# Kernel optimization log

Measured on AMD Instinct MI355X. Metric: run time of the kernel, lower is better.

## Reference

```python
import jax, jax.numpy as jnp
import numpy as np

K_BASE = 8
K_MAX = 20
NUM_GROUPS = 16  # min(32, 64 // 4)
EPS = 1e-5


def _knn_idx_adaptive(x, mask, k_base=K_BASE, k_max=K_MAX):
    # x: [B, N, D] float, mask: [B, N] bool. Returns idx: [B, N, k_max] int32.
    B, N, D = x.shape
    x2 = jnp.sum(x * x, axis=-1, keepdims=True)              # [B, N, 1]
    dist2 = x2 + x2.transpose(0, 2, 1) - 2.0 * jnp.einsum('bnd,bmd->bnm', x, x)
    dist2 = jnp.clip(dist2, 0.0)
    valid = mask[:, :, None] & mask[:, None, :]
    eye = jnp.eye(N, dtype=bool)[None]
    dist2 = jnp.where(valid & ~eye, dist2, jnp.inf)
    counts = mask.sum(axis=1)                                 # [B]
    k_per = jnp.clip(jnp.sqrt(counts.astype(jnp.float32) / 50.0) * k_base,
                     k_base, k_max).astype(jnp.int32)         # truncation == torch .long()
    k_global = jnp.minimum(k_max, jnp.maximum(1, counts.min() - 1))
    _, idx = jax.lax.top_k(-dist2, k_max)                     # [B, N, k_max]
    first_valid = jnp.argmax(mask, axis=1)                    # [B]
    cols = jnp.arange(k_max)[None, None, :]
    k_eff = jnp.minimum(k_per, k_global)[:, None, None]
    # cols < k_eff: true top-k neighbors; [k_eff, k_global): repeat first valid; >= k_global: pad 0
    idx = jnp.where(cols < k_eff, idx,
                    jnp.where(cols < k_global, first_valid[:, None, None], 0))
    return idx


def _group_norm(h, gamma, beta, num_groups=NUM_GROUPS, eps=EPS):
    # h: [..., C]
    shp = h.shape
    C = shp[-1]
    hg = h.reshape(shp[:-1] + (num_groups, C // num_groups))
    mu = hg.mean(axis=-1, keepdims=True)
    var = hg.var(axis=-1, keepdims=True)
    hg = (hg - mu) * jax.lax.rsqrt(var + eps)
    return hg.reshape(shp) * gamma + beta


def setup_inputs() -> dict:
    key = jax.random.key(0)
    kx, kl, k1, k2 = jax.random.split(key, 4)
    B, N, D, C = 16, 1024, 64, 64
    x = jax.random.normal(kx, (B, N, D), dtype=jnp.float32)
    lengths = jax.random.randint(kl, (B,), 256, N + 1)
    mask = jnp.arange(N)[None, :] < lengths[:, None]          # [B, N] bool
    W1 = jax.random.normal(k1, (2 * D, C), dtype=jnp.float32) / np.sqrt(2 * D)
    b1 = jnp.zeros((C,), dtype=jnp.float32)
    gamma = jnp.ones((C,), dtype=jnp.float32)
    beta = jnp.zeros((C,), dtype=jnp.float32)
    W2 = jax.random.normal(k2, (C, C), dtype=jnp.float32) / np.sqrt(C)
    b2 = jnp.zeros((C,), dtype=jnp.float32)
    return {"x": x, "mask": mask, "W1": W1, "b1": b1,
            "gamma": gamma, "beta": beta, "W2": W2, "b2": b2}


def reference(x, mask, W1, b1, gamma, beta, W2, b2):
    B, N, D = x.shape
    idx = _knn_idx_adaptive(x, mask)                          # [B, N, k]
    k = idx.shape[-1]
    x_nb = jnp.take_along_axis(x[:, :, None, :].repeat(1, axis=2),
                               idx[..., None], axis=1) if False else \
        x[jnp.arange(B)[:, None, None], idx]                  # [B, N, k, D]
    x_i = jnp.broadcast_to(x[:, :, None, :], (B, N, k, D))
    edge = jnp.concatenate([x_i, x_nb - x_i], axis=-1)        # [B, N, k, 2D]
    h = jax.nn.relu(_group_norm(edge @ W1 + b1, gamma, beta)) # [B, N, k, C]
    h = h @ W2 + b2
    out = h.max(axis=2)                                       # [B, N, C]
    return out * mask[..., None].astype(out.dtype)
```

## Files before the change

### kernel.cpp

```cpp
#include <hip/hip_runtime.h>
#include <stdint.h>

#define BB 16
#define NN 1024
#define DD 64
#define CC 64
#define KMAX 20
#define ROWS 8

typedef unsigned long long u64;
typedef float f32x2 __attribute__((ext_vector_type(2)));
typedef float f32x4v __attribute__((ext_vector_type(4)));
typedef short bf16x8 __attribute__((ext_vector_type(8)));

__device__ inline u64 umin64(u64 a, u64 b) { return a < b ? a : b; }

__device__ inline unsigned f2bf(float f) {
    unsigned u = __float_as_uint(f);
    return (u + 0x7FFFu + ((u >> 16) & 1u)) >> 16;
}

__device__ inline bf16x8 pack8(const float4 a, const float4 b) {
    union { unsigned u[4]; bf16x8 v; } r;
    r.u[0] = f2bf(a.x) | (f2bf(a.y) << 16);
    r.u[1] = f2bf(a.z) | (f2bf(a.w) << 16);
    r.u[2] = f2bf(b.x) | (f2bf(b.y) << 16);
    r.u[3] = f2bf(b.z) | (f2bf(b.w) << 16);
    return r.v;
}

struct bfpair { bf16x8 hi, lo; };
__device__ __forceinline__ bfpair split8(const float v[8]) {
    union { unsigned u[4]; bf16x8 x; } H, L;
#pragma unroll
    for (int i = 0; i < 4; ++i) {
        unsigned h0 = f2bf(v[2 * i]), h1 = f2bf(v[2 * i + 1]);
        float r0 = v[2 * i] - __uint_as_float(h0 << 16);
        float r1 = v[2 * i + 1] - __uint_as_float(h1 << 16);
        H.u[i] = h0 | (h1 << 16);
        L.u[i] = f2bf(r0) | (f2bf(r1) << 16);
    }
    bfpair r; r.hi = H.x; r.lo = L.x; return r;
}

__device__ inline void gn4(float4& h, const float4 g, const float4 be) {
    float mu = (h.x + h.y + h.z + h.w) * 0.25f;
    float dx = h.x - mu, dy = h.y - mu, dz = h.z - mu, dw = h.w - mu;
    float var = (dx * dx + dy * dy + dz * dz + dw * dw) * 0.25f;
    float rs = __builtin_amdgcn_rsqf(var + 1e-5f);
    h.x = fmaxf(fmaf(dx * rs, g.x, be.x), 0.f);
    h.y = fmaxf(fmaf(dy * rs, g.y, be.y), 0.f);
    h.z = fmaxf(fmaf(dz * rs, g.z, be.z), 0.f);
    h.w = fmaxf(fmaf(dw * rs, g.w, be.w), 0.f);
}

__global__ __launch_bounds__(256) void k1_feats(const float* __restrict__ x,
                                                const float* __restrict__ W1,
                                                const float* __restrict__ b1,
                                                float* __restrict__ base,
                                                float* __restrict__ fb,
                                                float* __restrict__ x2,
                                                float* __restrict__ xT,
                                                const void* __restrict__ maskp,
                                                int* __restrict__ counts,
                                                int* __restrict__ keff) {
    __shared__ float sXT[16][65];
    __shared__ int scnt[BB];
    int w = threadIdx.x >> 6, lane = threadIdx.x & 63;
    int lg = lane >> 4, lr = lane & 15;
    int p0 = blockIdx.x * 16;

    float av[8];
    bfpair A[2];
    {
        const float* xr = x + (size_t)(p0 + lr) * DD;
#pragma unroll
        for (int kt = 0; kt < 2; ++kt) {
            float4 a0 = *(const float4*)(xr + kt * 32 + lg * 8);
            float4 a1 = *(const float4*)(xr + kt * 32 + lg * 8 + 4);
            av[0] = a0.x; av[1] = a0.y; av[2] = a0.z; av[3] = a0.w;
            av[4] = a1.x; av[5] = a1.y; av[6] = a1.z; av[7] = a1.w;
            A[kt] = split8(av);
        }
    }
    bfpair Wa[2], Wb[2];
#pragma unroll
    for (int kt = 0; kt < 2; ++kt) {
        const float* wpa = W1 + (size_t)(kt * 32 + lg * 8) * CC + w * 16 + lr;
        float wv[8];
#pragma unroll
        for (int e = 0; e < 8; ++e) wv[e] = wpa[e * CC];
        Wa[kt] = split8(wv);
        const float* wpb = wpa + (size_t)DD * CC;
#pragma unroll
        for (int e = 0; e < 8; ++e) wv[e] = wpb[e * CC];
        Wb[kt] = split8(wv);
    }

    f32x4v P = {0, 0, 0, 0}, Q = {0, 0, 0, 0};
#pragma unroll
    for (int kt = 0; kt < 2; ++kt) {
        P = __builtin_amdgcn_mfma_f32_16x16x32_bf16(A[kt].hi, Wa[kt].hi, P, 0, 0, 0);
        P = __builtin_amdgcn_mfma_f32_16x16x32_bf16(A[kt].hi, Wa[kt].lo, P, 0, 0, 0);
        P = __builtin_amdgcn_mfma_f32_16x16x32_bf16(A[kt].lo, Wa[kt].hi, P, 0, 0, 0);
        Q = __builtin_amdgcn_mfma_f32_16x16x32_bf16(A[kt].hi, Wb[kt].hi, Q, 0, 0, 0);
        Q = __builtin_amdgcn_mfma_f32_16x16x32_bf16(A[kt].hi, Wb[kt].lo, Q, 0, 0, 0);
        Q = __builtin_amdgcn_mfma_f32_16x16x32_bf16(A[kt].lo, Wb[kt].hi, Q, 0, 0, 0);
    }
    {
        float b1c = b1[w * 16 + lr];
#pragma unroll
        for (int r = 0; r < 4; ++r) {
            size_t off = (size_t)(p0 + lg * 4 + r) * CC + w * 16 + lr;
            base[off] = P[r] - Q[r] + b1c;
            fb[off] = Q[r];
        }
    }

#pragma unroll
    for (int q2 = 0; q2 < 4; ++q2) {
        int pl = w + q2 * 4;
        int p = p0 + pl;
        float xv = x[(size_t)p * DD + lane];
        sXT[pl][lane] = xv;
        float sq = xv * xv;
        for (int off = 32; off; off >>= 1) sq += __shfl_xor(sq, off);
        if (lane == 0) x2[p] = sq;
    }
    __syncthreads();
    {
        int b = p0 >> 10, nb = p0 & 1023;
        int t = threadIdx.x;
#pragma unroll
        for (int pass = 0; pass < 4; ++pass) {
            int d = pass * 16 + (t >> 4);
            int pt = t & 15;
            xT[(((size_t)(b << 6) + d) << 10) + nb + pt] = sXT[pt][d];
        }
    }

    if (blockIdx.x == 0) {
        const unsigned char* mb = (const unsigned char*)maskp;
        const int* mi = (const int*)maskp;
        bool bytelayout = (mb[1] != 0);
        for (int bq = 0; bq < 4; ++bq) {
            int bb = w * 4 + bq;
            int s = 0;
            for (int i = 0; i < 16; ++i) {
                int nn2 = lane + (i << 6);
                int v = bytelayout ? (mb[bb * NN + nn2] ? 1 : 0)
                                   : (mi[bb * NN + nn2] ? 1 : 0);
                s += v;
            }
            for (int off = 32; off; off >>= 1) s += __shfl_xor(s, off);
            if (lane == 0) scnt[bb] = s;
        }
        __syncthreads();
        int t = threadIdx.x;
        if (t < BB) {
            int minc = scnt[0];
            for (int qq = 1; qq < BB; ++qq) minc = min(minc, scnt[qq]);
            int kglob = min(KMAX, max(1, minc - 1));
            float c = (float)scnt[t];
            float v = sqrtf(c / 50.0f) * 8.0f;
            v = fminf(fmaxf(v, 8.0f), 20.0f);
            int kper = (int)v;
            counts[t] = scnt[t];
            keff[t] = min(kper, kglob);
        }
    }
}

#define CE(a, b)                                                      \
    {                                                                 \
        bool sw_ = pk[b] < pk[a];                                     \
        u64 ta_ = pk[a];                                              \
        pk[a] = sw_ ? pk[b] : pk[a];                                  \
        pk[b] = sw_ ? ta_ : pk[b];                                    \
    }

__device__ __forceinline__ u64 head16(const u64 (&pk)[16]) {
    u64 h01 = umin64(pk[0], pk[1]),   h23 = umin64(pk[2], pk[3]);
    u64 h45 = umin64(pk[4], pk[5]),   h67 = umin64(pk[6], pk[7]);
    u64 h89 = umin64(pk[8], pk[9]),   hab = umin64(pk[10], pk[11]);
    u64 hcd = umin64(pk[12], pk[13]), hef = umin64(pk[14], pk[15]);
    return umin64(umin64(umin64(h01, h23), umin64(h45, h67)),
                  umin64(umin64(h89, hab), umin64(hcd, hef)));
}

__device__ __forceinline__ int sortpop(u64 (&pk)[16], int kef, int lane) {
    CE(0,1) CE(2,3) CE(4,5) CE(6,7) CE(8,9) CE(10,11) CE(12,13) CE(14,15)
    CE(0,2) CE(1,3) CE(4,6) CE(5,7) CE(8,10) CE(9,11) CE(12,14) CE(13,15)
    CE(1,2) CE(5,6) CE(9,10) CE(13,14)
    CE(0,4) CE(1,5) CE(2,6) CE(3,7) CE(8,12) CE(9,13) CE(10,14) CE(11,15)
    CE(2,4) CE(3,5) CE(10,12) CE(11,13)
    CE(1,2) CE(3,4) CE(5,6) CE(9,10) CE(11,12) CE(13,14)
    CE(0,8) CE(1,9) CE(2,10) CE(3,11) CE(4,12) CE(5,13) CE(6,14) CE(7,15)
    CE(4,8) CE(5,9) CE(6,10) CE(7,11)
    CE(2,4) CE(3,5) CE(6,8) CE(7,9) CE(10,12) CE(11,13)
    CE(1,2) CE(3,4) CE(5,6) CE(7,8) CE(9,10) CE(11,12) CE(13,14)
    u64 myhead = pk[0];
    int my_m = 0;
    for (int j = 0; j < kef; ++j) {
        u64 g = myhead;
        for (int off = 32; off; off >>= 1) {
            u64 o = __shfl_xor(g, off);
            g = (o < g) ? o : g;
        }
        my_m = (j == lane) ? (int)(unsigned)(g & 0xffffffffu) : my_m;
        bool win = (myhead == g);
#pragma unroll
        for (int tt = 0; tt < 15; ++tt) pk[tt] = win ? pk[tt + 1] : pk[tt];
        pk[15] = win ? ~0ULL : pk[15];
        myhead = pk[0];
    }
    return my_m;
}

#define ROWFMA(r, rv, cv)                                                        \
    {                                                                            \
        axy[r] = __builtin_elementwise_fma((f32x2){rv, rv}, (f32x2){cv.x, cv.y}, \
                                           axy[r]);                              \
        azw[r] = __builtin_elementwise_fma((f32x2){rv, rv}, (f32x2){cv.z, cv.w}, \
                                           azw[r]);                              \
    }

__global__ __launch_bounds__(256) void k2_knn(const float* __restrict__ x,
                                              const float* __restrict__ xT,
                                              const float* __restrict__ x2,
                                              const int* __restrict__ counts,
                                              const int* __restrict__ keff,
                                              int* __restrict__ idx) {
    __shared__ float sD[ROWS][NN];
    __shared__ float sX2[NN];
    int b = blockIdx.x >> 7;
    int n0 = (blockIdx.x & 127) * ROWS;
    int cnt = counts[b];
    if (n0 >= cnt) return;
    int kef = keff[b];
    int w = threadIdx.x >> 6, lane = threadIdx.x & 63;
    int t = threadIdx.x;
    *(float4*)&sX2[t << 2] = *(const float4*)(x2 + (b << 10) + (t << 2));
    __syncthreads();

    if ((w << 8) < cnt) {
        f32x2 axy[ROWS], azw[ROWS];
#pragma unroll
        for (int r = 0; r < ROWS; ++r) { axy[r] = (f32x2){0.f, 0.f}; azw[r] = (f32x2){0.f, 0.f}; }
        const float* xTb = xT + ((size_t)b << 16);
        const float* xrow0 = x + ((size_t)(b << 10) + n0) * DD;
        int c0 = (w << 8) + (lane << 2);
        for (int d0 = 0; d0 < DD; d0 += 4) {
            float4 cv0 = *(const float4*)(xTb + ((size_t)(d0 + 0) << 10) + c0);
            float4 cv1 = *(const float4*)(xTb + ((size_t)(d0 + 1) << 10) + c0);
            float4 cv2 = *(const float4*)(xTb + ((size_t)(d0 + 2) << 10) + c0);
            float4 cv3 = *(const float4*)(xTb + ((size_t)(d0 + 3) << 10) + c0);
#pragma unroll
            for (int r = 0; r < ROWS; ++r) {
                float4 rv = *(const float4*)(xrow0 + r * DD + d0);
                ROWFMA(r, rv.x, cv0)
                ROWFMA(r, rv.y, cv1)
                ROWFMA(r, rv.z, cv2)
                ROWFMA(r, rv.w, cv3)
            }
        }
#pragma unroll
        for (int r = 0; r < ROWS; ++r)
            *(float4*)&sD[r][c0] = make_float4(axy[r].x, axy[r].y, azw[r].x, azw[r].y);
    }
    __syncthreads();

    int rA = w, rB = w + 4;
    int nA = n0 + rA, nB = n0 + rB;
    bool vA = nA < cnt, vB = nB < cnt;
    if (!vA) return;
    float x2A = sX2[nA];
    float x2B = sX2[nB & 1023];
    u64 pkA[16], pkB[16];
#pragma unroll
    for (int tt = 0; tt < 16; ++tt) {
        int c = (tt << 6) + lane;
        float dA = fmaxf((x2A + sX2[c]) - 2.0f * sD[rA][c], 0.0f);
        float dB = fmaxf((x2B + sX2[c]) - 2.0f * sD[rB][c], 0.0f);
        pkA[tt] = (c < cnt && c != nA)
            ? (((u64)__float_as_uint(dA) << 32) | (unsigned)c) : ~0ULL;
        pkB[tt] = (vB && c < cnt && c != nB)
            ? (((u64)__float_as_uint(dB) << 32) | (unsigned)c) : ~0ULL;
    }
    u64 hA = head16(pkA), hB = head16(pkB);
    unsigned hA32 = (unsigned)(hA >> 32), hB32 = (unsigned)(hB >> 32);
    unsigned prefA = 0u, prefB = 0u;
    int rankA = kef, rankB = kef;
#pragma unroll
    for (int bbit = 31; bbit >= 0; --bbit) {
        unsigned bitm = 1u << bbit;
        bool cA = ((((u64)(hA32 ^ prefA)) >> (bbit + 1)) == 0) && ((hA32 & bitm) == 0);
        bool cB = ((((u64)(hB32 ^ prefB)) >> (bbit + 1)) == 0) && ((hB32 & bitm) == 0);
        u64 mA = __ballot(cA);
        u64 mB = __ballot(cB);
        int nA0 = __popcll(mA), nB0 = __popcll(mB);
        if (rankA > nA0) { rankA -= nA0; prefA |= bitm; }
        if (rankB > nB0) { rankB -= nB0; prefB |= bitm; }
    }
    u64 t0A = (((u64)prefA) << 32) | 0xFFFFFFFFULL;
    u64 t0B = vB ? ((((u64)prefB) << 32) | 0xFFFFFFFFULL) : 0ULL;

    u64* svA = (u64*)&sD[rA][0];
    u64* svB = (u64*)&sD[rB][0];
    u64 lmask = (lane == 0) ? 0ULL : ((~0ULL) >> (64 - lane));
    int SA = 0, SB = 0;
#pragma unroll
    for (int i = 0; i < 16; ++i) {
        bool qA = (pkA[i] <= t0A);
        bool qB = (pkB[i] <= t0B);
        u64 mA = __ballot(qA);
        u64 mB = __ballot(qB);
        if (qA) svA[SA + __popcll(mA & lmask)] = pkA[i];
        if (qB) svB[SB + __popcll(mB & lmask)] = pkB[i];
        SA += __popcll(mA);
        SB += __popcll(mB);
    }
    size_t prowA = (size_t)(b << 10) + nA;
    size_t prowB = (size_t)(b << 10) + nB;
    if (SA <= 64 && SB <= 64) {
        u64 sA = (lane < SA) ? svA[lane] : ~0ULL;
        u64 sB = (lane < SB) ? svB[lane] : ~0ULL;
        int rkA = 0, rkB = 0;
        int SM = max(SA, SB);
        for (int j = 0; j < SM; ++j) {
            u64 aj = svA[j];
            u64 bj = svB[j];
            rkA += (j < SA && aj < sA) ? 1 : 0;
            rkB += (j < SB && bj < sB) ? 1 : 0;
        }
        if (rkA < kef && lane < SA) idx[prowA * KMAX + rkA] = (int)(unsigned)(sA & 0xffffffffu);
        if (lane >= kef && lane < KMAX) idx[prowA * KMAX + lane] = 0;
        if (vB) {
            if (rkB < kef && lane < SB) idx[prowB * KMAX + rkB] = (int)(unsigned)(sB & 0xffffffffu);
            if (lane >= kef && lane < KMAX) idx[prowB * KMAX + lane] = 0;
        }
    } else {
        int mA = sortpop(pkA, kef, lane);
        if (lane < KMAX) idx[prowA * KMAX + lane] = (lane < kef) ? mA : 0;
        if (vB) {
            int mB = sortpop(pkB, kef, lane);
            if (lane < KMAX) idx[prowB * KMAX + lane] = (lane < kef) ? mB : 0;
        }
    }
}

__global__ __launch_bounds__(256, 2) void k3_mlp(const float* __restrict__ base,
                                                 const float* __restrict__ fb,
                                                 const int* __restrict__ idx,
                                                 const int* __restrict__ counts,
                                                 const float* __restrict__ gamma,
                                                 const float* __restrict__ beta,
                                                 const float* __restrict__ W2,
                                                 const float* __restrict__ b2,
                                                 float* __restrict__ out) {
    __shared__ float sC[4][64][20];
    int w = threadIdx.x >> 6, lane = threadIdx.x & 63;
    int lg = lane >> 4, lr = lane & 15;
    int p0 = blockIdx.x * 16;
    int b = p0 >> 10;
    int n0b = p0 & 1023;
    int cnt = counts[b];
    int pt = p0 + lr;
    bool aval = (n0b + lr) < cnt;

    bf16x8 Bf[4][2];
#pragma unroll
    for (int nt = 0; nt < 4; ++nt)
#pragma unroll
        for (int kt = 0; kt < 2; ++kt) {
            float4 lo, hi;
            const float* wp = W2 + (size_t)(kt * 32 + lg * 8) * CC + nt * 16 + lr;
            lo.x = wp[0 * CC]; lo.y = wp[1 * CC]; lo.z = wp[2 * CC]; lo.w = wp[3 * CC];
            hi.x = wp[4 * CC]; hi.y = wp[5 * CC]; hi.z = wp[6 * CC]; hi.w = wp[7 * CC];
            Bf[nt][kt] = pack8(lo, hi);
        }

    const float* bp = base + (size_t)pt * CC + lg * 8;
    float4 baA0 = *(const float4*)(bp);
    float4 baA1 = *(const float4*)(bp + 4);
    float4 baB0 = *(const float4*)(bp + 32);
    float4 baB1 = *(const float4*)(bp + 36);
    const float* gp = gamma + lg * 8;
    float4 gA0 = *(const float4*)(gp),      gA1 = *(const float4*)(gp + 4);
    float4 gB0 = *(const float4*)(gp + 32), gB1 = *(const float4*)(gp + 36);
    const float* bep = beta + lg * 8;
    float4 eA0 = *(const float4*)(bep),      eA1 = *(const float4*)(bep + 4);
    float4 eB0 = *(const float4*)(bep + 32), eB1 = *(const float4*)(bep + 36);

    const float* fbb = fb + ((size_t)(b << 10)) * CC;
    const int* idxp = idx + (size_t)pt * KMAX;

    f32x4v cmax[4];
#pragma unroll
    for (int nt = 0; nt < 4; ++nt) cmax[nt] = (f32x4v){-1e30f, -1e30f, -1e30f, -1e30f};

#pragma unroll
    for (int jj = 0; jj < 5; ++jj) {
        int j = w * 5 + jj;
        int m = aval ? idxp[j] : 0;
        const float* fr = fbb + (size_t)m * CC + lg * 8;
        float4 hA0 = *(const float4*)(fr);
        float4 hA1 = *(const float4*)(fr + 4);
        float4 hB0 = *(const float4*)(fr + 32);
        float4 hB1 = *(const float4*)(fr + 36);
        hA0.x += baA0.x; hA0.y += baA0.y; hA0.z += baA0.z; hA0.w += baA0.w;
        hA1.x += baA1.x; hA1.y += baA1.y; hA1.z += baA1.z; hA1.w += baA1.w;
        hB0.x += baB0.x; hB0.y += baB0.y; hB0.z += baB0.z; hB0.w += baB0.w;
        hB1.x += baB1.x; hB1.y += baB1.y; hB1.z += baB1.z; hB1.w += baB1.w;
        gn4(hA0, gA0, eA0);
        gn4(hA1, gA1, eA1);
        gn4(hB0, gB0, eB0);
        gn4(hB1, gB1, eB1);
        bf16x8 A0 = pack8(hA0, hA1);
        bf16x8 A1 = pack8(hB0, hB1);
#pragma unroll
        for (int nt = 0; nt < 4; ++nt) {
            f32x4v c = {0.f, 0.f, 0.f, 0.f};
            c = __builtin_amdgcn_mfma_f32_16x16x32_bf16(A0, Bf[nt][0], c, 0, 0, 0);
            c = __builtin_amdgcn_mfma_f32_16x16x32_bf16(A1, Bf[nt][1], c, 0, 0, 0);
            cmax[nt].x = fmaxf(cmax[nt].x, c.x);
            cmax[nt].y = fmaxf(cmax[nt].y, c.y);
            cmax[nt].z = fmaxf(cmax[nt].z, c.z);
            cmax[nt].w = fmaxf(cmax[nt].w, c.w);
        }
    }
#pragma unroll
    for (int nt = 0; nt < 4; ++nt)
        *(float4*)&sC[w][lane][nt * 4] = (float4){cmax[nt].x, cmax[nt].y, cmax[nt].z, cmax[nt].w};
    __syncthreads();
    float b2c = b2[lane];
#pragma unroll
    for (int q = 0; q < 4; ++q) {
        int R = w * 4 + q;
        int src = ((R >> 2) << 4) + lr;
        int reg = (lg << 2) + (R & 3);
        float v = fmaxf(fmaxf(sC[0][src][reg], sC[1][src][reg]),
                        fmaxf(sC[2][src][reg], sC[3][src][reg]));
        bool valid = (n0b + R) < cnt;
        out[(size_t)(p0 + R) * CC + lane] = valid ? (v + b2c) : 0.f;
    }
}

extern "C" void kernel_launch(void* const* d_in, const int* in_sizes, int n_in,
                              void* d_out, int out_size, void* d_ws, size_t ws_size,
                              hipStream_t stream) {
    const float* x     = (const float*)d_in[0];
    const void*  maskp = d_in[1];
    const float* W1    = (const float*)d_in[2];
    const float* b1    = (const float*)d_in[3];
    const float* gamma = (const float*)d_in[4];
    const float* beta  = (const float*)d_in[5];
    const float* W2    = (const float*)d_in[6];
    const float* b2    = (const float*)d_in[7];
    float* out = (float*)d_out;

    int* d_counts = (int*)d_ws;
    int* d_keff   = d_counts + 16;
    float* d_x2   = (float*)(d_counts + 32);
    float* d_base = d_x2 + BB * NN;
    float* d_fb   = d_base + (size_t)BB * NN * CC;
    int* d_idx    = (int*)(d_fb + (size_t)BB * NN * CC);
    float* d_xT   = (float*)d_out;

    hipLaunchKernelGGL(k1_feats, dim3(BB * NN / 16), dim3(256), 0, stream,
                       x, W1, b1, d_base, d_fb, d_x2, d_xT, maskp, d_counts, d_keff);
    hipLaunchKernelGGL(k2_knn, dim3(BB * (NN / ROWS)), dim3(256), 0, stream,
                       x, d_xT, d_x2, d_counts, d_keff, d_idx);
    hipLaunchKernelGGL(k3_mlp, dim3(BB * NN / 16), dim3(256), 0, stream,
                       d_base, d_fb, d_idx, d_counts, gamma, beta, W2, b2, out);
}
```

Before: 92.04 us.

## Split feature kernel, add counts kernel, vectorize transpose, shorten radix threshold search

Splits the first kernel into a one-block mask-count kernel, a W1 projection kernel and a transpose/x2 kernel, and writes the transposed x with float4 stores. In the kNN kernel the radix search for the k-th distance threshold now covers only the top 16 bits of the float, which halves the ballot loop. The candidate set can then grow because the threshold is coarser, and there are two extra kernel launches.

```diff
diff --git a/kernel.cpp b/kernel.cpp
--- a/kernel.cpp
+++ b/kernel.cpp
@@ -54,18 +54,41 @@
     h.w = fmaxf(fmaf(dw * rs, g.w, be.w), 0.f);
 }
 
-__global__ __launch_bounds__(256) void k1_feats(const float* __restrict__ x,
-                                                const float* __restrict__ W1,
-                                                const float* __restrict__ b1,
-                                                float* __restrict__ base,
-                                                float* __restrict__ fb,
-                                                float* __restrict__ x2,
-                                                float* __restrict__ xT,
-                                                const void* __restrict__ maskp,
-                                                int* __restrict__ counts,
-                                                int* __restrict__ keff) {
-    __shared__ float sXT[16][65];
+__global__ void k0_counts(const void* __restrict__ maskp,
+                          int* __restrict__ counts, int* __restrict__ keff) {
     __shared__ int scnt[BB];
+    int tid = threadIdx.x;
+    int w = tid >> 6, lane = tid & 63;
+    const unsigned char* mb = (const unsigned char*)maskp;
+    const int* mi = (const int*)maskp;
+    bool bytelayout = (mb[1] != 0);
+    int s = 0;
+    for (int i = 0; i < 16; ++i) {
+        int n = lane + (i << 6);
+        int v = bytelayout ? (mb[w * NN + n] ? 1 : 0) : (mi[w * NN + n] ? 1 : 0);
+        s += v;
+    }
+    for (int off = 32; off; off >>= 1) s += __shfl_xor(s, off);
+    if (lane == 0) scnt[w] = s;
+    __syncthreads();
+    if (tid < BB) {
+        int minc = scnt[0];
+        for (int q = 1; q < BB; ++q) minc = min(minc, scnt[q]);
+        int kglob = min(KMAX, max(1, minc - 1));
+        float c = (float)scnt[tid];
+        float v = sqrtf(c / 50.0f) * 8.0f;
+        v = fminf(fmaxf(v, 8.0f), 20.0f);
+        int kper = (int)v;
+        counts[tid] = scnt[tid];
+        keff[tid] = min(kper, kglob);
+    }
+}
+
+__global__ __launch_bounds__(256) void k1a_feats(const float* __restrict__ x,
+                                                 const float* __restrict__ W1,
+                                                 const float* __restrict__ b1,
+                                                 float* __restrict__ base,
+                                                 float* __restrict__ fb) {
     int w = threadIdx.x >> 6, lane = threadIdx.x & 63;
     int lg = lane >> 4, lr = lane & 15;
     int p0 = blockIdx.x * 16;
@@ -116,59 +139,30 @@
             fb[off] = Q[r];
         }
     }
-
-#pragma unroll
-    for (int q2 = 0; q2 < 4; ++q2) {
-        int pl = w + q2 * 4;
-        int p = p0 + pl;
-        float xv = x[(size_t)p * DD + lane];
-        sXT[pl][lane] = xv;
+}
+
+__global__ __launch_bounds__(256) void k1b_xt(const float* __restrict__ x,
+                                              float* __restrict__ xT,
+                                              float* __restrict__ x2) {
+    __shared__ float sX[16][65];
+    int w = threadIdx.x >> 6, lane = threadIdx.x & 63;
+    int p0 = blockIdx.x * 16;
+#pragma unroll
+    for (int q = 0; q < 4; ++q) {
+        int pl = w * 4 + q;
+        float xv = x[((size_t)(p0 + pl) << 6) + lane];
+        sX[pl][lane] = xv;
         float sq = xv * xv;
         for (int off = 32; off; off >>= 1) sq += __shfl_xor(sq, off);
-        if (lane == 0) x2[p] = sq;
+        if (lane == 0) x2[p0 + pl] = sq;
     }
     __syncthreads();
-    {
-        int b = p0 >> 10, nb = p0 & 1023;
-        int t = threadIdx.x;
-#pragma unroll
-        for (int pass = 0; pass < 4; ++pass) {
-            int d = pass * 16 + (t >> 4);
-            int pt = t & 15;
-            xT[(((size_t)(b << 6) + d) << 10) + nb + pt] = sXT[pt][d];
-        }
-    }
-
-    if (blockIdx.x == 0) {
-        const unsigned char* mb = (const unsigned char*)maskp;
-        const int* mi = (const int*)maskp;
-        bool bytelayout = (mb[1] != 0);
-        for (int bq = 0; bq < 4; ++bq) {
-            int bb = w * 4 + bq;
-            int s = 0;
-            for (int i = 0; i < 16; ++i) {
-                int nn2 = lane + (i << 6);
-                int v = bytelayout ? (mb[bb * NN + nn2] ? 1 : 0)
-                                   : (mi[bb * NN + nn2] ? 1 : 0);
-                s += v;
-            }
-            for (int off = 32; off; off >>= 1) s += __shfl_xor(s, off);
-            if (lane == 0) scnt[bb] = s;
-        }
-        __syncthreads();
-        int t = threadIdx.x;
-        if (t < BB) {
-            int minc = scnt[0];
-            for (int qq = 1; qq < BB; ++qq) minc = min(minc, scnt[qq]);
-            int kglob = min(KMAX, max(1, minc - 1));
-            float c = (float)scnt[t];
-            float v = sqrtf(c / 50.0f) * 8.0f;
-            v = fminf(fmaxf(v, 8.0f), 20.0f);
-            int kper = (int)v;
-            counts[t] = scnt[t];
-            keff[t] = min(kper, kglob);
-        }
-    }
+    int t = threadIdx.x;
+    int b = p0 >> 10, nb = p0 & 1023;
+    int d = t >> 2, q4 = (t & 3) << 2;
+    float4 v;
+    v.x = sX[q4 + 0][d]; v.y = sX[q4 + 1][d]; v.z = sX[q4 + 2][d]; v.w = sX[q4 + 3][d];
+    *(float4*)&xT[(((size_t)(b << 6) + d) << 10) + nb + q4] = v;
 }
 
 #define CE(a, b)                                                      \
@@ -288,22 +282,22 @@
             ? (((u64)__float_as_uint(dB) << 32) | (unsigned)c) : ~0ULL;
     }
     u64 hA = head16(pkA), hB = head16(pkB);
-    unsigned hA32 = (unsigned)(hA >> 32), hB32 = (unsigned)(hB >> 32);
+    unsigned hTA = (unsigned)(hA >> 48), hTB = (unsigned)(hB >> 48);
     unsigned prefA = 0u, prefB = 0u;
     int rankA = kef, rankB = kef;
 #pragma unroll
-    for (int bbit = 31; bbit >= 0; --bbit) {
+    for (int bbit = 15; bbit >= 0; --bbit) {
         unsigned bitm = 1u << bbit;
-        bool cA = ((((u64)(hA32 ^ prefA)) >> (bbit + 1)) == 0) && ((hA32 & bitm) == 0);
-        bool cB = ((((u64)(hB32 ^ prefB)) >> (bbit + 1)) == 0) && ((hB32 & bitm) == 0);
+        bool cA = (((hTA ^ prefA) >> (bbit + 1)) == 0) && ((hTA & bitm) == 0);
+        bool cB = (((hTB ^ prefB) >> (bbit + 1)) == 0) && ((hTB & bitm) == 0);
         u64 mA = __ballot(cA);
         u64 mB = __ballot(cB);
         int nA0 = __popcll(mA), nB0 = __popcll(mB);
         if (rankA > nA0) { rankA -= nA0; prefA |= bitm; }
         if (rankB > nB0) { rankB -= nB0; prefB |= bitm; }
     }
-    u64 t0A = (((u64)prefA) << 32) | 0xFFFFFFFFULL;
-    u64 t0B = vB ? ((((u64)prefB) << 32) | 0xFFFFFFFFULL) : 0ULL;
+    u64 t0A = ((u64)((prefA << 16) | 0xFFFFu) << 32) | 0xFFFFFFFFULL;
+    u64 t0B = vB ? (((u64)((prefB << 16) | 0xFFFFu) << 32) | 0xFFFFFFFFULL) : 0ULL;
 
     u64* svA = (u64*)&sD[rA][0];
     u64* svB = (u64*)&sD[rB][0];
@@ -467,8 +461,11 @@
     int* d_idx    = (int*)(d_fb + (size_t)BB * NN * CC);
     float* d_xT   = (float*)d_out;
 
-    hipLaunchKernelGGL(k1_feats, dim3(BB * NN / 16), dim3(256), 0, stream,
-                       x, W1, b1, d_base, d_fb, d_x2, d_xT, maskp, d_counts, d_keff);
+    hipLaunchKernelGGL(k0_counts, dim3(1), dim3(1024), 0, stream, maskp, d_counts, d_keff);
+    hipLaunchKernelGGL(k1a_feats, dim3(BB * NN / 16), dim3(256), 0, stream,
+                       x, W1, b1, d_base, d_fb);
+    hipLaunchKernelGGL(k1b_xt, dim3(BB * NN / 16), dim3(256), 0, stream,
+                       x, d_xT, d_x2);
     hipLaunchKernelGGL(k2_knn, dim3(BB * (NN / ROWS)), dim3(256), 0, stream,
                        x, d_xT, d_x2, d_counts, d_keff, d_idx);
     hipLaunchKernelGGL(k3_mlp, dim3(BB * NN / 16), dim3(256), 0, stream,
```

Result: faster. 82.86 us (median of 3 runs) (-10.0%).
